# Optimization experiments

Measured on AMD Instinct MI355X. Metric: run time of the kernel, lower is better.

Reference implementation:

```python
import jax, jax.numpy as jnp
import numpy as np

N, E, D, H = 50000, 800000, 128, 4
HD = D // H          # head_dim = 32
K = 1.0              # Lorentz manifold curvature parameter k


def setup_inputs() -> dict:
    key = jax.random.key(0)
    ks = jax.random.split(key, 8)
    # valid points on the hyperboloid: time = sqrt(|space|^2 + k)
    xs = jax.random.normal(ks[0], (N, D), dtype=jnp.float32) * 0.1
    xt = jnp.sqrt(jnp.sum(xs * xs, -1, keepdims=True) + K)
    x = jnp.concatenate([xt, xs], -1)                      # [N, D+1]
    edge_index = jax.random.randint(ks[1], (2, E), 0, N)   # [2, E] (src, dst)
    s = 0.05
    Wq = jax.random.normal(ks[2], (H, HD, D + 1), dtype=jnp.float32) * s
    Wk = jax.random.normal(ks[3], (H, HD, D + 1), dtype=jnp.float32) * s
    Wv = jax.random.normal(ks[4], (H, HD, D + 1), dtype=jnp.float32) * s
    Wo = jax.random.normal(ks[5], (D, D + 1), dtype=jnp.float32) * s
    bq = jnp.zeros((H, HD), jnp.float32)
    bk = jnp.zeros((H, HD), jnp.float32)
    bv = jnp.zeros((H, HD), jnp.float32)
    bo = jnp.zeros((D,), jnp.float32)
    return dict(x=x, edge_index=edge_index, Wq=Wq, bq=bq, Wk=Wk, bk=bk,
                Wv=Wv, bv=bv, Wo=Wo, bo=bo)


def _time(space):
    return jnp.sqrt(jnp.sum(space * space, -1, keepdims=True) + K)


def _hyp_linear_heads(x, W, b):
    # x:[N,D+1], W:[H,HD,D+1] -> [N,H,HD+1] (all heads in one einsum)
    space = jnp.einsum('nd,hod->nho', x, W) + b
    return jnp.concatenate([_time(space), space], -1)


def _hyp_linear(x, W, b):
    # x:[N,D+1], W:[D,D+1] -> [N,D+1]
    space = jnp.einsum('nd,od->no', x, W) + b
    return jnp.concatenate([_time(space), space], -1)


def _cinner(a, b):
    # Lorentz inner product: -a0*b0 + <a_s, b_s>
    return jnp.sum(a * b, -1) - 2.0 * a[..., 0] * b[..., 0]


def reference(x, edge_index, Wq, bq, Wk, bk, Wv, bv, Wo, bo):
    src, dst = edge_index[0], edge_index[1]
    q = _hyp_linear_heads(x, Wq, bq)   # [N,H,HD+1]
    k = _hyp_linear_heads(x, Wk, bk)
    v = _hyp_linear_heads(x, Wv, bv)
    # per-edge Lorentz attention scores [E,H]
    scores = (2.0 + 2.0 * _cinner(q[dst], k[src])) / np.sqrt(HD).astype(np.float32)
    # scatter softmax grouped by dst
    m = jax.ops.segment_max(scores, dst, num_segments=N)      # [N,H]
    e = jnp.exp(scores - m[dst])
    ssum = jax.ops.segment_sum(e, dst, num_segments=N)        # [N,H]
    attn = e / ssum[dst]                                      # [E,H]
    # Lorentz weighted midpoint aggregation
    agg = jax.ops.segment_sum(attn[..., None] * v[src], dst, num_segments=N)  # [N,H,HD+1]
    denom = jnp.sqrt(jnp.clip(jnp.abs(_cinner(agg, agg)), 1e-8, None))[..., None]
    out = np.sqrt(K).astype(np.float32) * agg / denom          # [N,H,HD+1]
    # drop per-head time coords, merge heads, recompute time
    out_space = out[..., 1:].reshape(N, D)
    out = jnp.concatenate([_time(out_space), out_space], -1)   # [N,D+1]
    return _hyp_linear(out, Wo, bo)
```

## Files before the change

### kernel.cpp

```cpp
#include <hip/hip_runtime.h>
#include <hip/hip_bf16.h>
#include <math.h>


__global__ void prep_kernel(const float* __restrict__ Wq, const float* __restrict__ bq,
                            const float* __restrict__ Wk, const float* __restrict__ bk,
                            const float* __restrict__ Wv, const float* __restrict__ bv,
                            const float* __restrict__ Wo,
                            float* __restrict__ WT, float* __restrict__ bias,
                            float* __restrict__ WoT) {
    const int T1 = 129 * 384;
    const int T2 = T1 + 384;
    const int T3 = T2 + 129 * 128;
    for (int i = blockIdx.x * blockDim.x + threadIdx.x; i < T3; i += gridDim.x * blockDim.x) {
        if (i < T1) {
            int k = i / 384, o = i % 384;
            const float* W = (o < 128) ? Wq : (o < 256 ? Wk : Wv);
            int r = o & 127;
            WT[i] = W[(size_t)r * 129 + k];
        } else if (i < T2) {
            int o = i - T1;
            const float* b = (o < 128) ? bq : (o < 256 ? bk : bv);
            bias[o] = b[o & 127];
        } else {
            int j = i - T2;
            int k = j >> 7, o = j & 127;
            WoT[j] = Wo[(size_t)o * 129 + k];
        }
    }
}

__global__ __launch_bounds__(256) void qkv_gemm(const float* __restrict__ x,
                                                const float* __restrict__ WT,
                                                const float* __restrict__ bias,
                                                float* __restrict__ qh, float* __restrict__ kv,
                                                float* __restrict__ tvec, int Nn) {
    __shared__ __align__(16) float xs[16][132];
    __shared__ __align__(16) float ws[16][132];
    int tid = threadIdx.x;
    int tx = tid & 15, ty = tid >> 4;
    int nbase = blockIdx.x * 128;
    int cbase = blockIdx.y * 128;

    float acc[8][8];
#pragma unroll
    for (int i = 0; i < 8; i++)
#pragma unroll
        for (int j = 0; j < 8; j++) acc[i][j] = 0.f;

    for (int k0 = 0; k0 < 129; k0 += 16) {
#pragma unroll
        for (int it = 0; it < 8; it++) {
            int i = tid + it * 256;
            int kk = i & 15, r = i >> 4;
            int n = nbase + r, k = k0 + kk;
            xs[kk][r] = (n < Nn && k < 129) ? x[(size_t)n * 129 + k] : 0.f;
        }
#pragma unroll
        for (int it = 0; it < 2; it++) {
            int i = tid + it * 256;
            int c4 = i & 31, kk = i >> 5;
            int k = k0 + kk;
            float4 wv = {0.f, 0.f, 0.f, 0.f};
            if (k < 129) wv = *(const float4*)&WT[(size_t)k * 384 + cbase + c4 * 4];
            *(float4*)&ws[kk][c4 * 4] = wv;
        }
        __syncthreads();
#pragma unroll
        for (int kk = 0; kk < 16; kk++) {
            float4 a0 = *(const float4*)&xs[kk][ty * 8];
            float4 a1 = *(const float4*)&xs[kk][ty * 8 + 4];
            float4 b0 = *(const float4*)&ws[kk][tx * 8];
            float4 b1 = *(const float4*)&ws[kk][tx * 8 + 4];
            float av[8] = {a0.x, a0.y, a0.z, a0.w, a1.x, a1.y, a1.z, a1.w};
            float bw[8] = {b0.x, b0.y, b0.z, b0.w, b1.x, b1.y, b1.z, b1.w};
#pragma unroll
            for (int i = 0; i < 8; i++)
#pragma unroll
                for (int j = 0; j < 8; j++) acc[i][j] = fmaf(av[i], bw[j], acc[i][j]);
        }
        __syncthreads();
    }

    int t = blockIdx.y;
    int hh = tx >> 2;
    float4 bb0 = *(const float4*)&bias[cbase + tx * 8];
    float4 bb1 = *(const float4*)&bias[cbase + tx * 8 + 4];
#pragma unroll
    for (int i = 0; i < 8; i++) {
        int n = nbase + ty * 8 + i;
        float4 lo, hi;
        lo.x = acc[i][0] + bb0.x;
        lo.y = acc[i][1] + bb0.y;
        lo.z = acc[i][2] + bb0.z;
        lo.w = acc[i][3] + bb0.w;
        hi.x = acc[i][4] + bb1.x;
        hi.y = acc[i][5] + bb1.y;
        hi.z = acc[i][6] + bb1.z;
        hi.w = acc[i][7] + bb1.w;
        float s = lo.x * lo.x + lo.y * lo.y + lo.z * lo.z + lo.w * lo.w +
                  hi.x * hi.x + hi.y * hi.y + hi.z * hi.z + hi.w * hi.w;
        s += __shfl_xor(s, 1);
        s += __shfl_xor(s, 2);
        if (n < Nn) {
            if (t == 0) {
                *(float4*)&qh[(size_t)n * 128 + tx * 8] = lo;
                *(float4*)&qh[(size_t)n * 128 + tx * 8 + 4] = hi;
                if ((tx & 3) == 0) tvec[n * 16 + 8 + hh] = sqrtf(s + 1.0f);
            } else if (t == 1) {
                *(float4*)&kv[(size_t)n * 256 + tx * 8] = lo;
                *(float4*)&kv[(size_t)n * 256 + tx * 8 + 4] = hi;
                if ((tx & 3) == 0) tvec[n * 16 + hh] = sqrtf(s + 1.0f);
            } else {
                *(float4*)&kv[(size_t)n * 256 + 128 + tx * 8] = lo;
                *(float4*)&kv[(size_t)n * 256 + 128 + tx * 8 + 4] = hi;
                if ((tx & 3) == 0) tvec[n * 16 + 4 + hh] = sqrtf(s + 1.0f);
            }
        }
    }
}

__global__ void count_kernel(const int* __restrict__ ei, int* __restrict__ deg, int E) {
    int e = blockIdx.x * blockDim.x + threadIdx.x;
    if (e < E) atomicAdd(&deg[ei[E + e]], 1);
}

__global__ __launch_bounds__(256) void scan_blocks(const int* __restrict__ deg,
                                                   int* __restrict__ offsets,
                                                   int* __restrict__ partials, int n) {
    __shared__ int wsum[4];
    int tid = threadIdx.x;
    int idx = blockIdx.x * 256 + tid;
    int lane = tid & 63, wid = tid >> 6;
    int v = (idx < n) ? deg[idx] : 0;
    int x = v;
#pragma unroll
    for (int d = 1; d < 64; d <<= 1) {
        int y = __shfl_up(x, d, 64);
        if (lane >= d) x += y;
    }
    if (lane == 63) wsum[wid] = x;
    __syncthreads();
    if (tid == 0) {
        int s = 0;
#pragma unroll
        for (int i = 0; i < 4; i++) { int tv = wsum[i]; wsum[i] = s; s += tv; }
    }
    __syncthreads();
    int excl = wsum[wid] + x - v;
    if (idx < n) offsets[idx] = excl;
    if (tid == 255) partials[blockIdx.x] = excl + v;
}

__global__ __launch_bounds__(256) void scan_partials(int* __restrict__ partials,
                                                     int* __restrict__ total_out, int nb) {
    __shared__ int wsum[4];
    int tid = threadIdx.x;
    int lane = tid & 63, wid = tid >> 6;
    int v = (tid < nb) ? partials[tid] : 0;
    int x = v;
#pragma unroll
    for (int d = 1; d < 64; d <<= 1) {
        int y = __shfl_up(x, d, 64);
        if (lane >= d) x += y;
    }
    if (lane == 63) wsum[wid] = x;
    __syncthreads();
    if (tid == 0) {
        int s = 0;
#pragma unroll
        for (int i = 0; i < 4; i++) { int tv = wsum[i]; wsum[i] = s; s += tv; }
    }
    __syncthreads();
    int excl = wsum[wid] + x - v;
    if (tid < nb) partials[tid] = excl;
    if (tid == 255) *total_out = excl + v;
}

__global__ void scan_add(int* __restrict__ offsets, const int* __restrict__ partials, int n) {
    int idx = blockIdx.x * blockDim.x + threadIdx.x;
    if (idx < n) offsets[idx] += partials[blockIdx.x];
}

__global__ void fill_kernel(const int* __restrict__ ei, const int* __restrict__ offsets,
                            int* __restrict__ cursor, int* __restrict__ srcs, int E) {
    int e = blockIdx.x * blockDim.x + threadIdx.x;
    if (e < E) {
        int src = ei[e];
        int dst = ei[E + e];
        int pos = atomicAdd(&cursor[dst], 1);
        srcs[offsets[dst] + pos] = src * 256;
    }
}

__global__ __launch_bounds__(256) void attn_kernel(const float* __restrict__ qh,
                                                   const float* __restrict__ kv,
                                                   const float* __restrict__ tvec,
                                                   const int* __restrict__ offsets,
                                                   const int* __restrict__ soff,
                                                   float* __restrict__ mid, int Nn) {
    int tid = threadIdx.x;
    int n = (blockIdx.x * blockDim.x + tid) >> 6;
    if (n >= Nn) return;
    int lw = tid & 63;
    int t = lw >> 4;
    int l = lw & 15;
    int base = lw & 48;
    int ha = l >> 3;

    float4 qa = *(const float4*)&qh[(size_t)n * 128 + l * 4];
    float4 qb = *(const float4*)&qh[(size_t)n * 128 + 64 + l * 4];
    float qta = tvec[n * 16 + 8 + ha];
    float qtb = tvec[n * 16 + 10 + ha];

    float4 acc_a = {0.f, 0.f, 0.f, 0.f}, acc_b = {0.f, 0.f, 0.f, 0.f};
    float acc_ta = 0.f, acc_tb = 0.f;

    int r0 = offsets[n], r1 = offsets[n + 1];
    int e = r0 + t;
    int off = (e < r1) ? soff[e] : 0;
    for (; e < r1; e += 4) {
        int offn = (e + 4 < r1) ? soff[e + 4] : 0;
        const float* row = kv + off;
        float4 k0 = *(const float4*)&row[l * 4];
        float4 k1 = *(const float4*)&row[64 + l * 4];
        float4 v0 = *(const float4*)&row[128 + l * 4];
        float4 v1 = *(const float4*)&row[192 + l * 4];
        float tv = tvec[(off >> 4) + (l & 7)];

        float pa = qa.x * k0.x + qa.y * k0.y + qa.z * k0.z + qa.w * k0.w;
        float pb = qb.x * k1.x + qb.y * k1.y + qb.z * k1.z + qb.w * k1.w;
        pa += __shfl_xor(pa, 1);
        pb += __shfl_xor(pb, 1);
        pa += __shfl_xor(pa, 2);
        pb += __shfl_xor(pb, 2);
        pa += __shfl_xor(pa, 4);
        pb += __shfl_xor(pb, 4);
        float kta = __shfl(tv, base + ha);
        float ktb = __shfl(tv, base + 2 + ha);
        float vta = __shfl(tv, base + 4 + ha);
        float vtb = __shfl(tv, base + 6 + ha);
        float sa = (1.0f + pa - qta * kta) * 0.35355339059327373f;
        float sb = (1.0f + pb - qtb * ktb) * 0.35355339059327373f;
        float wa = __expf(sa), wb = __expf(sb);
        acc_a.x += wa * v0.x; acc_a.y += wa * v0.y; acc_a.z += wa * v0.z; acc_a.w += wa * v0.w;
        acc_b.x += wb * v1.x; acc_b.y += wb * v1.y; acc_b.z += wb * v1.z; acc_b.w += wb * v1.w;
        acc_ta = fmaf(wa, vta, acc_ta);
        acc_tb = fmaf(wb, vtb, acc_tb);
        off = offn;
    }

#define MRG(x) x += __shfl_xor(x, 16); x += __shfl_xor(x, 32);
    MRG(acc_a.x) MRG(acc_a.y) MRG(acc_a.z) MRG(acc_a.w)
    MRG(acc_b.x) MRG(acc_b.y) MRG(acc_b.z) MRG(acc_b.w)
    MRG(acc_ta) MRG(acc_tb)
#undef MRG

    float ssa = acc_a.x * acc_a.x + acc_a.y * acc_a.y + acc_a.z * acc_a.z + acc_a.w * acc_a.w;
    float ssb = acc_b.x * acc_b.x + acc_b.y * acc_b.y + acc_b.z * acc_b.z + acc_b.w * acc_b.w;
    ssa += __shfl_xor(ssa, 1);
    ssb += __shfl_xor(ssb, 1);
    ssa += __shfl_xor(ssa, 2);
    ssb += __shfl_xor(ssb, 2);
    ssa += __shfl_xor(ssa, 4);
    ssb += __shfl_xor(ssb, 4);
    float ca = ssa - acc_ta * acc_ta;
    float cb = ssb - acc_tb * acc_tb;
    float inva = 1.0f / sqrtf(fmaxf(fabsf(ca), 1e-8f));
    float invb = 1.0f / sqrtf(fmaxf(fabsf(cb), 1e-8f));

    if (t == 0) {
        float4 oa = {acc_a.x * inva, acc_a.y * inva, acc_a.z * inva, acc_a.w * inva};
        float4 ob = {acc_b.x * invb, acc_b.y * invb, acc_b.z * invb, acc_b.w * invb};
        *(float4*)&mid[(size_t)n * 128 + l * 4] = oa;
        *(float4*)&mid[(size_t)n * 128 + 64 + l * 4] = ob;
    }
}

__global__ __launch_bounds__(128) void final_linear(const float* __restrict__ mid,
                                                    const float* __restrict__ WoT,
                                                    const float* __restrict__ bo,
                                                    float* __restrict__ out, int Nn) {
    __shared__ __align__(16) float xl[32][132];
    int tid = threadIdx.x;
    int nb = blockIdx.x * 32;
#pragma unroll
    for (int i = 0; i < 32; i++) {
        int n = nb + i;
        xl[i][1 + tid] = (n < Nn) ? mid[(size_t)n * 128 + tid] : 0.f;
    }
    __syncthreads();
    int nl = tid >> 2, sub = tid & 3;
    {
        float s = 0.f;
#pragma unroll
        for (int j = 0; j < 32; j++) {
            float v = xl[nl][1 + sub * 32 + j];
            s += v * v;
        }
        s += __shfl_xor(s, 1);
        s += __shfl_xor(s, 2);
        if (sub == 0) xl[nl][0] = sqrtf(s + 1.0f);
    }
    __syncthreads();

    float bv = bo[tid];
    float acc[32];
#pragma unroll
    for (int i = 0; i < 32; i++) acc[i] = bv;

    for (int k = 0; k < 128; k += 4) {
        float w0 = WoT[(size_t)(k + 0) * 128 + tid];
        float w1 = WoT[(size_t)(k + 1) * 128 + tid];
        float w2 = WoT[(size_t)(k + 2) * 128 + tid];
        float w3 = WoT[(size_t)(k + 3) * 128 + tid];
#pragma unroll
        for (int i = 0; i < 32; i++) {
            float4 xv = *(const float4*)&xl[i][k];
            acc[i] += w0 * xv.x + w1 * xv.y + w2 * xv.z + w3 * xv.w;
        }
    }
    {
        float w = WoT[(size_t)128 * 128 + tid];
#pragma unroll
        for (int i = 0; i < 32; i++) acc[i] += w * xl[i][128];
    }
    __syncthreads();
#pragma unroll
    for (int i = 0; i < 32; i++) {
        int n = nb + i;
        if (n < Nn) out[(size_t)n * 129 + 1 + tid] = acc[i];
        xl[i][tid] = acc[i] * acc[i];
    }
    __syncthreads();
    {
        float s = 0.f;
#pragma unroll
        for (int j = 0; j < 32; j++) s += xl[nl][sub * 32 + j];
        s += __shfl_xor(s, 1);
        s += __shfl_xor(s, 2);
        if (sub == 0 && (nb + nl) < Nn) out[(size_t)(nb + nl) * 129] = sqrtf(s + 1.0f);
    }
}

__global__ __launch_bounds__(1024) void scan_kernel(const int* __restrict__ deg,
                                                    int* __restrict__ offsets, int n) {
    __shared__ int wsum[16];
    __shared__ int carry_s;
    int tid = threadIdx.x;
    int lane = tid & 63, wid = tid >> 6;
    if (tid == 0) carry_s = 0;
    __syncthreads();
    for (int base = 0; base < n; base += 1024) {
        int idx = base + tid;
        int v = (idx < n) ? deg[idx] : 0;
        int x = v;
#pragma unroll
        for (int d = 1; d < 64; d <<= 1) {
            int y = __shfl_up(x, d, 64);
            if (lane >= d) x += y;
        }
        if (lane == 63) wsum[wid] = x;
        __syncthreads();
        if (wid == 0) {
            int s = (lane < 16) ? wsum[lane] : 0;
#pragma unroll
            for (int d = 1; d < 16; d <<= 1) {
                int y = __shfl_up(s, d, 64);
                if (lane >= d) s += y;
            }
            if (lane < 16) wsum[lane] = s;
        }
        __syncthreads();
        int waveoff = (wid > 0) ? wsum[wid - 1] : 0;
        int excl = carry_s + waveoff + x - v;
        if (idx < n) offsets[idx] = excl;
        __syncthreads();
        if (tid == 0) carry_s += wsum[15];
        __syncthreads();
    }
    if (tid == 0) offsets[n] = carry_s;
}

extern "C" void kernel_launch(void* const* d_in, const int* in_sizes, int n_in,
                              void* d_out, int out_size, void* d_ws, size_t ws_size,
                              hipStream_t stream) {
    const float* x  = (const float*)d_in[0];
    const int*   ei = (const int*)d_in[1];
    const float* Wq = (const float*)d_in[2];
    const float* bq = (const float*)d_in[3];
    const float* Wk = (const float*)d_in[4];
    const float* bk = (const float*)d_in[5];
    const float* Wv = (const float*)d_in[6];
    const float* bv = (const float*)d_in[7];
    const float* Wo = (const float*)d_in[8];
    const float* bo = (const float*)d_in[9];
    float* out = (float*)d_out;

    const int N = in_sizes[0] / 129;
    const int E = in_sizes[1] / 2;

    char* w = (char*)d_ws;
    size_t off = 0;
    auto alloc = [&](size_t bytes) {
        void* p = w + off;
        off += (bytes + 255) & ~(size_t)255;
        return p;
    };
    float* qh       = (float*)alloc((size_t)N * 128 * 4);
    float* kv       = (float*)alloc((size_t)N * 256 * 4);
    float* tvec     = (float*)alloc((size_t)N * 16 * 4);
    float* mid      = (float*)alloc((size_t)N * 128 * 4);
    float* WT       = (float*)alloc(129 * 384 * 4);
    float* bias     = (float*)alloc(384 * 4);
    float* WoT      = (float*)alloc(129 * 128 * 4);
    int*   offsets  = (int*)alloc((size_t)(N + 1) * 4);
    int*   degcur   = (int*)alloc((size_t)2 * N * 4);
    int*   deg      = degcur;
    int*   cursor   = degcur + N;
    int*   partials = (int*)alloc(256 * 4);
    int*   srcs     = (int*)alloc((size_t)E * 4);

    hipMemsetAsync(degcur, 0, (size_t)2 * N * 4, stream);

    prep_kernel<<<260, 256, 0, stream>>>(Wq, bq, Wk, bk, Wv, bv, Wo, WT, bias, WoT);

    dim3 g1((N + 127) / 128, 3);
    qkv_gemm<<<g1, 256, 0, stream>>>(x, WT, bias, qh, kv, tvec, N);

    count_kernel<<<(E + 255) / 256, 256, 0, stream>>>(ei, deg, E);

    int nb = (N + 255) / 256;
    if (nb <= 256) {
        scan_blocks<<<nb, 256, 0, stream>>>(deg, offsets, partials, N);
        scan_partials<<<1, 256, 0, stream>>>(partials, offsets + N, nb);
        scan_add<<<nb, 256, 0, stream>>>(offsets, partials, N);
    } else {
        scan_kernel<<<1, 1024, 0, stream>>>(deg, offsets, N);
    }

    fill_kernel<<<(E + 255) / 256, 256, 0, stream>>>(ei, offsets, cursor, srcs, E);

    attn_kernel<<<(N + 3) / 4, 256, 0, stream>>>(qh, kv, tvec, offsets, srcs, mid, N);

    final_linear<<<(N + 31) / 32, 128, 0, stream>>>(mid, WoT, bo, out, N);
}
```

Measured before the change: 459.4 us.

## Store K/V in bf16, recompute time coords in attention, pre-transpose x

K and V projections are now written as packed bf16, halving the bytes gathered per edge in the attention kernel. The separate time-coordinate buffer is dropped; the attention kernel recomputes q, k and v time components from squared norms with extra shuffles and sqrt per edge. A transpose kernel turns x into k-major layout so the QKV GEMM can load x tiles with float4 reads. The trade-off is reduced precision on K/V, one extra pass over x, and more ALU work per edge.

```diff
diff --git a/kernel.cpp b/kernel.cpp
--- a/kernel.cpp
+++ b/kernel.cpp
@@ -2,6 +2,16 @@
 #include <hip/hip_bf16.h>
 #include <math.h>
 
+
+typedef unsigned int uint32;
+typedef unsigned short ushort16;
+
+__device__ __forceinline__ float lo16(uint32 u) { return __uint_as_float(u << 16); }
+__device__ __forceinline__ float hi16(uint32 u) { return __uint_as_float(u & 0xFFFF0000u); }
+__device__ __forceinline__ uint32 f2bf(float f) {
+    uint32 u = __float_as_uint(f);
+    return (u + 0x7FFFu + ((u >> 16) & 1u)) >> 16;
+}
 
 __global__ void prep_kernel(const float* __restrict__ Wq, const float* __restrict__ bq,
                             const float* __restrict__ Wk, const float* __restrict__ bk,
@@ -30,11 +40,32 @@
     }
 }
 
-__global__ __launch_bounds__(256) void qkv_gemm(const float* __restrict__ x,
+__global__ __launch_bounds__(256) void xpose(const float* __restrict__ x,
+                                             float* __restrict__ xT, int Nn) {
+    __shared__ float tile[32][33];
+    int n0 = blockIdx.x * 32;
+    int k0 = blockIdx.y * 32;
+    int tx = threadIdx.x & 31, ty = threadIdx.x >> 5;
+#pragma unroll
+    for (int i = 0; i < 4; i++) {
+        int nl = ty + i * 8;
+        int n = n0 + nl, k = k0 + tx;
+        tile[nl][tx] = (n < Nn && k < 129) ? x[(size_t)n * 129 + k] : 0.f;
+    }
+    __syncthreads();
+#pragma unroll
+    for (int i = 0; i < 4; i++) {
+        int kl = ty + i * 8;
+        int k = k0 + kl, n = n0 + tx;
+        if (k < 129 && n < Nn) xT[(size_t)k * Nn + n] = tile[tx][kl];
+    }
+}
+
+__global__ __launch_bounds__(256) void qkv_gemm(const float* __restrict__ xT,
                                                 const float* __restrict__ WT,
                                                 const float* __restrict__ bias,
-                                                float* __restrict__ qh, float* __restrict__ kv,
-                                                float* __restrict__ tvec, int Nn) {
+                                                float* __restrict__ qh,
+                                                ushort16* __restrict__ kvb, int Nn) {
     __shared__ __align__(16) float xs[16][132];
     __shared__ __align__(16) float ws[16][132];
     int tid = threadIdx.x;
@@ -50,11 +81,23 @@
 
     for (int k0 = 0; k0 < 129; k0 += 16) {
 #pragma unroll
-        for (int it = 0; it < 8; it++) {
-            int i = tid + it * 256;
-            int kk = i & 15, r = i >> 4;
-            int n = nbase + r, k = k0 + kk;
-            xs[kk][r] = (n < Nn && k < 129) ? x[(size_t)n * 129 + k] : 0.f;
+        for (int it = 0; it < 2; it++) {
+            int j = tid + it * 256;
+            int kk = j >> 5, c4 = j & 31;
+            int k = k0 + kk, n0 = nbase + c4 * 4;
+            float4 xv = {0.f, 0.f, 0.f, 0.f};
+            if (k < 129) {
+                if (n0 + 4 <= Nn) {
+                    xv = *(const float4*)&xT[(size_t)k * Nn + n0];
+                } else {
+                    const float* r = &xT[(size_t)k * Nn];
+                    if (n0 + 0 < Nn) xv.x = r[n0 + 0];
+                    if (n0 + 1 < Nn) xv.y = r[n0 + 1];
+                    if (n0 + 2 < Nn) xv.z = r[n0 + 2];
+                    if (n0 + 3 < Nn) xv.w = r[n0 + 3];
+                }
+            }
+            *(float4*)&xs[kk][c4 * 4] = xv;
         }
 #pragma unroll
         for (int it = 0; it < 2; it++) {
@@ -83,39 +126,28 @@
     }
 
     int t = blockIdx.y;
-    int hh = tx >> 2;
     float4 bb0 = *(const float4*)&bias[cbase + tx * 8];
     float4 bb1 = *(const float4*)&bias[cbase + tx * 8 + 4];
 #pragma unroll
     for (int i = 0; i < 8; i++) {
         int n = nbase + ty * 8 + i;
-        float4 lo, hi;
-        lo.x = acc[i][0] + bb0.x;
-        lo.y = acc[i][1] + bb0.y;
-        lo.z = acc[i][2] + bb0.z;
-        lo.w = acc[i][3] + bb0.w;
-        hi.x = acc[i][4] + bb1.x;
-        hi.y = acc[i][5] + bb1.y;
-        hi.z = acc[i][6] + bb1.z;
-        hi.w = acc[i][7] + bb1.w;
-        float s = lo.x * lo.x + lo.y * lo.y + lo.z * lo.z + lo.w * lo.w +
-                  hi.x * hi.x + hi.y * hi.y + hi.z * hi.z + hi.w * hi.w;
-        s += __shfl_xor(s, 1);
-        s += __shfl_xor(s, 2);
-        if (n < Nn) {
-            if (t == 0) {
-                *(float4*)&qh[(size_t)n * 128 + tx * 8] = lo;
-                *(float4*)&qh[(size_t)n * 128 + tx * 8 + 4] = hi;
-                if ((tx & 3) == 0) tvec[n * 16 + 8 + hh] = sqrtf(s + 1.0f);
-            } else if (t == 1) {
-                *(float4*)&kv[(size_t)n * 256 + tx * 8] = lo;
-                *(float4*)&kv[(size_t)n * 256 + tx * 8 + 4] = hi;
-                if ((tx & 3) == 0) tvec[n * 16 + hh] = sqrtf(s + 1.0f);
-            } else {
-                *(float4*)&kv[(size_t)n * 256 + 128 + tx * 8] = lo;
-                *(float4*)&kv[(size_t)n * 256 + 128 + tx * 8 + 4] = hi;
-                if ((tx & 3) == 0) tvec[n * 16 + 4 + hh] = sqrtf(s + 1.0f);
-            }
+        if (n >= Nn) continue;
+        float o[8];
+        o[0] = acc[i][0] + bb0.x; o[1] = acc[i][1] + bb0.y;
+        o[2] = acc[i][2] + bb0.z; o[3] = acc[i][3] + bb0.w;
+        o[4] = acc[i][4] + bb1.x; o[5] = acc[i][5] + bb1.y;
+        o[6] = acc[i][6] + bb1.z; o[7] = acc[i][7] + bb1.w;
+        if (t == 0) {
+            *(float4*)&qh[(size_t)n * 128 + tx * 8] = *(float4*)&o[0];
+            *(float4*)&qh[(size_t)n * 128 + tx * 8 + 4] = *(float4*)&o[4];
+        } else {
+            uint4 p;
+            p.x = f2bf(o[0]) | (f2bf(o[1]) << 16);
+            p.y = f2bf(o[2]) | (f2bf(o[3]) << 16);
+            p.z = f2bf(o[4]) | (f2bf(o[5]) << 16);
+            p.w = f2bf(o[6]) | (f2bf(o[7]) << 16);
+            int base = (t == 1) ? 0 : 128;
+            *(uint4*)&kvb[(size_t)n * 256 + base + tx * 8] = p;
         }
     }
 }
@@ -194,8 +226,7 @@
 }
 
 __global__ __launch_bounds__(256) void attn_kernel(const float* __restrict__ qh,
-                                                   const float* __restrict__ kv,
-                                                   const float* __restrict__ tvec,
+                                                   const ushort16* __restrict__ kvb,
                                                    const int* __restrict__ offsets,
                                                    const int* __restrict__ soff,
                                                    float* __restrict__ mid, int Nn) {
@@ -205,75 +236,80 @@
     int lw = tid & 63;
     int t = lw >> 4;
     int l = lw & 15;
-    int base = lw & 48;
-    int ha = l >> 3;
-
-    float4 qa = *(const float4*)&qh[(size_t)n * 128 + l * 4];
-    float4 qb = *(const float4*)&qh[(size_t)n * 128 + 64 + l * 4];
-    float qta = tvec[n * 16 + 8 + ha];
-    float qtb = tvec[n * 16 + 10 + ha];
-
-    float4 acc_a = {0.f, 0.f, 0.f, 0.f}, acc_b = {0.f, 0.f, 0.f, 0.f};
-    float acc_ta = 0.f, acc_tb = 0.f;
+
+    const float* qrow = qh + (size_t)n * 128 + l * 8;
+    float4 q0 = *(const float4*)qrow;
+    float4 q1 = *(const float4*)(qrow + 4);
+    float q2 = q0.x * q0.x + q0.y * q0.y + q0.z * q0.z + q0.w * q0.w +
+               q1.x * q1.x + q1.y * q1.y + q1.z * q1.z + q1.w * q1.w;
+    q2 += __shfl_xor(q2, 1);
+    q2 += __shfl_xor(q2, 2);
+    float qt = sqrtf(q2 + 1.0f);
+
+    float acc[8];
+#pragma unroll
+    for (int i = 0; i < 8; i++) acc[i] = 0.f;
+    float acct = 0.f;
 
     int r0 = offsets[n], r1 = offsets[n + 1];
     int e = r0 + t;
     int off = (e < r1) ? soff[e] : 0;
     for (; e < r1; e += 4) {
         int offn = (e + 4 < r1) ? soff[e + 4] : 0;
-        const float* row = kv + off;
-        float4 k0 = *(const float4*)&row[l * 4];
-        float4 k1 = *(const float4*)&row[64 + l * 4];
-        float4 v0 = *(const float4*)&row[128 + l * 4];
-        float4 v1 = *(const float4*)&row[192 + l * 4];
-        float tv = tvec[(off >> 4) + (l & 7)];
-
-        float pa = qa.x * k0.x + qa.y * k0.y + qa.z * k0.z + qa.w * k0.w;
-        float pb = qb.x * k1.x + qb.y * k1.y + qb.z * k1.z + qb.w * k1.w;
-        pa += __shfl_xor(pa, 1);
-        pb += __shfl_xor(pb, 1);
-        pa += __shfl_xor(pa, 2);
-        pb += __shfl_xor(pb, 2);
-        pa += __shfl_xor(pa, 4);
-        pb += __shfl_xor(pb, 4);
-        float kta = __shfl(tv, base + ha);
-        float ktb = __shfl(tv, base + 2 + ha);
-        float vta = __shfl(tv, base + 4 + ha);
-        float vtb = __shfl(tv, base + 6 + ha);
-        float sa = (1.0f + pa - qta * kta) * 0.35355339059327373f;
-        float sb = (1.0f + pb - qtb * ktb) * 0.35355339059327373f;
-        float wa = __expf(sa), wb = __expf(sb);
-        acc_a.x += wa * v0.x; acc_a.y += wa * v0.y; acc_a.z += wa * v0.z; acc_a.w += wa * v0.w;
-        acc_b.x += wb * v1.x; acc_b.y += wb * v1.y; acc_b.z += wb * v1.z; acc_b.w += wb * v1.w;
-        acc_ta = fmaf(wa, vta, acc_ta);
-        acc_tb = fmaf(wb, vtb, acc_tb);
+        const ushort16* row = kvb + off;
+        uint4 ku = *(const uint4*)(row + l * 8);
+        uint4 vu = *(const uint4*)(row + 128 + l * 8);
+
+        float kf[8] = {lo16(ku.x), hi16(ku.x), lo16(ku.y), hi16(ku.y),
+                       lo16(ku.z), hi16(ku.z), lo16(ku.w), hi16(ku.w)};
+        float vf[8] = {lo16(vu.x), hi16(vu.x), lo16(vu.y), hi16(vu.y),
+                       lo16(vu.z), hi16(vu.z), lo16(vu.w), hi16(vu.w)};
+        float qf[8] = {q0.x, q0.y, q0.z, q0.w, q1.x, q1.y, q1.z, q1.w};
+
+        float qk = 0.f, k2 = 0.f, v2 = 0.f;
+#pragma unroll
+        for (int j = 0; j < 8; j++) {
+            qk = fmaf(qf[j], kf[j], qk);
+            k2 = fmaf(kf[j], kf[j], k2);
+            v2 = fmaf(vf[j], vf[j], v2);
+        }
+        qk += __shfl_xor(qk, 1);
+        qk += __shfl_xor(qk, 2);
+        k2 += __shfl_xor(k2, 1);
+        k2 += __shfl_xor(k2, 2);
+        v2 += __shfl_xor(v2, 1);
+        v2 += __shfl_xor(v2, 2);
+        float kt = sqrtf(k2 + 1.0f);
+        float vt = sqrtf(v2 + 1.0f);
+        float s = (1.0f + qk - qt * kt) * 0.35355339059327373f;
+        float w = __expf(s);
+#pragma unroll
+        for (int j = 0; j < 8; j++) acc[j] = fmaf(w, vf[j], acc[j]);
+        acct = fmaf(w, vt, acct);
         off = offn;
     }
 
-#define MRG(x) x += __shfl_xor(x, 16); x += __shfl_xor(x, 32);
-    MRG(acc_a.x) MRG(acc_a.y) MRG(acc_a.z) MRG(acc_a.w)
-    MRG(acc_b.x) MRG(acc_b.y) MRG(acc_b.z) MRG(acc_b.w)
-    MRG(acc_ta) MRG(acc_tb)
-#undef MRG
-
-    float ssa = acc_a.x * acc_a.x + acc_a.y * acc_a.y + acc_a.z * acc_a.z + acc_a.w * acc_a.w;
-    float ssb = acc_b.x * acc_b.x + acc_b.y * acc_b.y + acc_b.z * acc_b.z + acc_b.w * acc_b.w;
-    ssa += __shfl_xor(ssa, 1);
-    ssb += __shfl_xor(ssb, 1);
-    ssa += __shfl_xor(ssa, 2);
-    ssb += __shfl_xor(ssb, 2);
-    ssa += __shfl_xor(ssa, 4);
-    ssb += __shfl_xor(ssb, 4);
-    float ca = ssa - acc_ta * acc_ta;
-    float cb = ssb - acc_tb * acc_tb;
-    float inva = 1.0f / sqrtf(fmaxf(fabsf(ca), 1e-8f));
-    float invb = 1.0f / sqrtf(fmaxf(fabsf(cb), 1e-8f));
+#pragma unroll
+    for (int j = 0; j < 8; j++) {
+        acc[j] += __shfl_xor(acc[j], 16);
+        acc[j] += __shfl_xor(acc[j], 32);
+    }
+    acct += __shfl_xor(acct, 16);
+    acct += __shfl_xor(acct, 32);
+
+    float ss = 0.f;
+#pragma unroll
+    for (int j = 0; j < 8; j++) ss = fmaf(acc[j], acc[j], ss);
+    ss += __shfl_xor(ss, 1);
+    ss += __shfl_xor(ss, 2);
+    float c = ss - acct * acct;
+    float inv = 1.0f / sqrtf(fmaxf(fabsf(c), 1e-8f));
 
     if (t == 0) {
-        float4 oa = {acc_a.x * inva, acc_a.y * inva, acc_a.z * inva, acc_a.w * inva};
-        float4 ob = {acc_b.x * invb, acc_b.y * invb, acc_b.z * invb, acc_b.w * invb};
-        *(float4*)&mid[(size_t)n * 128 + l * 4] = oa;
-        *(float4*)&mid[(size_t)n * 128 + 64 + l * 4] = ob;
+        float4 o0 = {acc[0] * inv, acc[1] * inv, acc[2] * inv, acc[3] * inv};
+        float4 o1 = {acc[4] * inv, acc[5] * inv, acc[6] * inv, acc[7] * inv};
+        *(float4*)&mid[(size_t)n * 128 + l * 8] = o0;
+        *(float4*)&mid[(size_t)n * 128 + l * 8 + 4] = o1;
     }
 }
 
@@ -407,26 +443,29 @@
         off += (bytes + 255) & ~(size_t)255;
         return p;
     };
-    float* qh       = (float*)alloc((size_t)N * 128 * 4);
-    float* kv       = (float*)alloc((size_t)N * 256 * 4);
-    float* tvec     = (float*)alloc((size_t)N * 16 * 4);
-    float* mid      = (float*)alloc((size_t)N * 128 * 4);
-    float* WT       = (float*)alloc(129 * 384 * 4);
-    float* bias     = (float*)alloc(384 * 4);
-    float* WoT      = (float*)alloc(129 * 128 * 4);
-    int*   offsets  = (int*)alloc((size_t)(N + 1) * 4);
-    int*   degcur   = (int*)alloc((size_t)2 * N * 4);
-    int*   deg      = degcur;
-    int*   cursor   = degcur + N;
-    int*   partials = (int*)alloc(256 * 4);
-    int*   srcs     = (int*)alloc((size_t)E * 4);
+    float*    qh       = (float*)alloc((size_t)N * 128 * 4);
+    ushort16* kvb      = (ushort16*)alloc((size_t)N * 256 * 2);
+    float*    xT       = (float*)alloc((size_t)129 * N * 4);
+    float*    mid      = (float*)alloc((size_t)N * 128 * 4);
+    float*    WT       = (float*)alloc(129 * 384 * 4);
+    float*    bias     = (float*)alloc(384 * 4);
+    float*    WoT      = (float*)alloc(129 * 128 * 4);
+    int*      offsets  = (int*)alloc((size_t)(N + 1) * 4);
+    int*      degcur   = (int*)alloc((size_t)2 * N * 4);
+    int*      deg      = degcur;
+    int*      cursor   = degcur + N;
+    int*      partials = (int*)alloc(256 * 4);
+    int*      srcs     = (int*)alloc((size_t)E * 4);
 
     hipMemsetAsync(degcur, 0, (size_t)2 * N * 4, stream);
 
     prep_kernel<<<260, 256, 0, stream>>>(Wq, bq, Wk, bk, Wv, bv, Wo, WT, bias, WoT);
 
+    dim3 gt((N + 31) / 32, 5);
+    xpose<<<gt, 256, 0, stream>>>(x, xT, N);
+
     dim3 g1((N + 127) / 128, 3);
-    qkv_gemm<<<g1, 256, 0, stream>>>(x, WT, bias, qh, kv, tvec, N);
+    qkv_gemm<<<g1, 256, 0, stream>>>(xT, WT, bias, qh, kvb, N);
 
     count_kernel<<<(E + 255) / 256, 256, 0, stream>>>(ei, deg, E);
 
@@ -441,7 +480,7 @@
 
     fill_kernel<<<(E + 255) / 256, 256, 0, stream>>>(ei, offsets, cursor, srcs, E);
 
-    attn_kernel<<<(N + 3) / 4, 256, 0, stream>>>(qh, kv, tvec, offsets, srcs, mid, N);
+    attn_kernel<<<(N + 3) / 4, 256, 0, stream>>>(qh, kvb, offsets, srcs, mid, N);
 
     final_linear<<<(N + 31) / 32, 128, 0, stream>>>(mid, WoT, bo, out, N);
 }
```

Result: faster. 376.7 us (-18.0%).
